# Kernel optimization log

Measured on AMD Instinct MI355X. Metric: run time of the kernel, lower is better.

## Reference

```python
import jax, jax.numpy as jnp
import numpy as np

N, C_IN, C, V = 500000, 64, 64, 20000  # C = out_channel // 2


def bn(x, g, b, eps):
    # training-mode BatchNorm1d: batch statistics, biased variance
    mu = jnp.mean(x, axis=0)
    var = jnp.mean(jnp.square(x - mu), axis=0)
    return (x - mu) * jax.lax.rsqrt(var + eps) * g + b


def setup_inputs() -> dict:
    key = jax.random.key(0)
    ks = jax.random.split(key, 12)
    s = 0.05
    return {
        "inputs": jax.random.normal(ks[0], (N, C_IN), jnp.float32),
        "unq_inv": jax.random.randint(ks[1], (N,), 0, V, jnp.int32),
        "kv_W": jax.random.normal(ks[2], (C_IN, C), jnp.float32) * s,
        "kv_b": jnp.zeros((C,), jnp.float32),
        "norm_g": jnp.ones((C,), jnp.float32),
        "norm_b": jnp.zeros((C,), jnp.float32),
        "w1_W": jax.random.normal(ks[3], (C_IN, C), jnp.float32) * s,
        "w1_bias": jnp.zeros((C,), jnp.float32),
        "w_bn_g": jnp.ones((C,), jnp.float32),
        "w_bn_b": jnp.zeros((C,), jnp.float32),
        "w2_W": jax.random.normal(ks[4], (C, C), jnp.float32) * s,
        "w2_bias": jnp.zeros((C,), jnp.float32),
        "pre_W": jax.random.normal(ks[5], (C_IN, C), jnp.float32) * s,
        "pre_bias": jnp.zeros((C,), jnp.float32),
        "pre_bn_g": jnp.ones((C,), jnp.float32),
        "pre_bn_b": jnp.zeros((C,), jnp.float32),
        "posw_W": jax.random.normal(ks[6], (C, C), jnp.float32) * s,
        "posw_bias": jnp.zeros((C,), jnp.float32),
        "link_bn_g": jnp.ones((C,), jnp.float32),
        "link_bn_b": jnp.zeros((C,), jnp.float32),
    }


def _forward(inputs, unq_inv, kv_W, kv_b, norm_g, norm_b, w1_W, w1_bias,
             w_bn_g, w_bn_b, w2_W, w2_bias, pre_W, pre_bias, pre_bn_g,
             pre_bn_b, posw_W, posw_bias, link_bn_g, link_bn_b):
    inv = unq_inv
    # v = kv(inputs); x = relu(norm(v))
    v = inputs @ kv_W + kv_b                                   # [N, C]
    x = jax.nn.relu(bn(v, norm_g, norm_b, 1e-3))               # [N, C]
    # scatter_max
    q_max = jax.ops.segment_max(x, inv, num_segments=V)        # [V, C]
    q_max = jnp.where(jnp.isneginf(q_max), 0.0, q_max)
    # weight = w(inputs): Linear -> BN -> ReLU -> Linear
    h = jax.nn.relu(bn(inputs @ w1_W + w1_bias, w_bn_g, w_bn_b, 1e-5))
    weight = h @ w2_W + w2_bias                                # [N, C]
    # scatter_softmax over segments
    m = jax.ops.segment_max(weight, inv, num_segments=V)
    m = jnp.where(jnp.isneginf(m), 0.0, m)
    ex = jnp.exp(weight - m[inv])
    denom = jax.ops.segment_sum(ex, inv, num_segments=V)
    soft_weight = ex / denom[inv]                              # [N, C]
    # scatter_mean(soft_weight * v)
    cnt = jax.ops.segment_sum(jnp.ones((inputs.shape[0],), inputs.dtype), inv, num_segments=V)
    cnt = jnp.maximum(cnt, 1.0)[:, None]
    weight_x = jax.ops.segment_sum(soft_weight * v, inv, num_segments=V) / cnt  # [V, C]
    # LinkConv(q_max, inputs, inv)
    p = bn(inputs @ pre_W + pre_bias, pre_bn_g, pre_bn_b, 1e-3)  # [N, C]
    pw = p @ posw_W + posw_bias
    fs = p * jnp.sin(pw)
    fc = p * jnp.cos(pw)
    add_s = jax.ops.segment_sum(fs, inv, num_segments=V)         # [V, C]
    add_c = jax.ops.segment_sum(fc, inv, num_segments=V)
    f = bn(q_max @ pre_W + pre_bias, pre_bn_g, pre_bn_b, 1e-3)   # [V, C]
    mw = f @ posw_W + posw_bias
    cs = f * jnp.sin(mw)
    cc = f * jnp.cos(mw)
    final = (add_s + cs) * cs + (add_c + cc) * cc
    link_feat = jax.nn.relu(bn(final, link_bn_g, link_bn_b, 1e-3))
    weight_x = (link_feat + weight_x) * 0.5
    return jnp.concatenate([weight_x, q_max], axis=-1)           # [V, 2C]


def reference(inputs, unq_inv, kv_W, kv_b, norm_g, norm_b, w1_W, w1_bias,
              w_bn_g, w_bn_b, w2_W, w2_bias, pre_W, pre_bias, pre_bn_g,
              pre_bn_b, posw_W, posw_bias, link_bn_g, link_bn_b):
    return _forward(inputs, unq_inv, kv_W, kv_b, norm_g, norm_b, w1_W, w1_bias,
                    w_bn_g, w_bn_b, w2_W, w2_bias, pre_W, pre_bias, pre_bn_g,
                    pre_bn_b, posw_W, posw_bias, link_bn_g, link_bn_b)
```

## Files before the change

kernel.cpp:

```cpp
#include <hip/hip_runtime.h>

typedef __attribute__((ext_vector_type(8))) short  bf16x8;
typedef __attribute__((ext_vector_type(4))) float  f32x4;

#define MFMA16(a,b,c) __builtin_amdgcn_mfma_f32_16x16x32_bf16((a),(b),(c),0,0,0)

__device__ __forceinline__ float b2f(ushort u){ return __uint_as_float(((unsigned)u)<<16); }
__device__ __forceinline__ ushort f2b(float f){
  unsigned u = __float_as_uint(f);
  unsigned r = (u + 0x7FFFu + ((u>>16)&1u)) >> 16;
  return (ushort)r;
}
__device__ __forceinline__ float ldv(const void* p, long i, int mode){
  return mode ? ((const float*)p)[i] : b2f(((const ushort*)p)[i]);
}

__global__ void pfn_detect(const void* X, int* mode){
  __shared__ int cnt;
  if (threadIdx.x==0) cnt=0;
  __syncthreads();
  const ushort* u = (const ushort*)X;
  int bad=0;
  for (int i=threadIdx.x; i<4096; i+=256){
    float v = b2f(u[i]);
    if (!(fabsf(v) < 1e4f)) bad++;
  }
  atomicAdd(&cnt, bad);
  __syncthreads();
  if (threadIdx.x==0) *mode = (cnt > 204) ? 1 : 0;
}

__global__ __launch_bounds__(256) void pfn_g(const void* __restrict__ X, int N,
                                             float* __restrict__ G, float* __restrict__ svec,
                                             const int* gmode,
                                             const int* __restrict__ inv, int* __restrict__ hist, int V)
{
  __shared__ __align__(16) ushort xt[128*72];
  __shared__ float gred[4096];
  __shared__ float sred[64];
  int mode = *gmode;
  int tid = threadIdx.x;
  int w = tid>>6, lane = tid&63, q = lane>>4, li = lane&15;

  {
    long i = (long)blockIdx.x*blockDim.x + tid;
    long stride = (long)gridDim.x*blockDim.x;
    for (; i<N; i+=stride){
      int s = min(max(inv[i],0), V-1);
      atomicAdd(&hist[s], 1);
    }
  }

  for (int u=tid; u<4096; u+=256) gred[u]=0.f;
  if (tid<64) sred[tid]=0.f;

  float s_acc[32];
#pragma unroll
  for (int i=0;i<32;i++) s_acc[i]=0.f;
  const f32x4 fz = {0.f,0.f,0.f,0.f};
  f32x4 acc[4][4];
#pragma unroll
  for (int a=0;a<4;a++)
#pragma unroll
    for (int b=0;b<4;b++) acc[a][b]=fz;

  int rr = tid>>1, half = tid&1;
  int nch = (N + 127)/128;
  for (int cb = blockIdx.x; cb < nch; cb += gridDim.x){
    int r = cb*128 + rr;
    uint4* dst = (uint4*)(xt + rr*72 + half*32);
    if (r < N){
      if (mode){
        const float4* src = (const float4*)((const float*)X + (size_t)r*64 + half*32);
#pragma unroll
        for (int i=0;i<4;i++){
          float4 f0=src[i*2], f1=src[i*2+1];
          s_acc[i*8+0]+=f0.x; s_acc[i*8+1]+=f0.y; s_acc[i*8+2]+=f0.z; s_acc[i*8+3]+=f0.w;
          s_acc[i*8+4]+=f1.x; s_acc[i*8+5]+=f1.y; s_acc[i*8+6]+=f1.z; s_acc[i*8+7]+=f1.w;
          uint4 u;
          u.x = (unsigned)f2b(f0.x) | ((unsigned)f2b(f0.y)<<16);
          u.y = (unsigned)f2b(f0.z) | ((unsigned)f2b(f0.w)<<16);
          u.z = (unsigned)f2b(f1.x) | ((unsigned)f2b(f1.y)<<16);
          u.w = (unsigned)f2b(f1.z) | ((unsigned)f2b(f1.w)<<16);
          dst[i]=u;
        }
      } else {
        const uint4* src = (const uint4*)((const ushort*)X + (size_t)r*64 + half*32);
#pragma unroll
        for (int i=0;i<4;i++){
          uint4 u=src[i]; dst[i]=u;
          const ushort* pu=(const ushort*)&u;
#pragma unroll
          for (int l=0;l<8;l++) s_acc[i*8+l] += b2f(pu[l]);
        }
      }
    } else {
      uint4 z={0,0,0,0};
#pragma unroll
      for (int i=0;i<4;i++) dst[i]=z;
    }
    __syncthreads();

    bf16x8 fr[4];
#pragma unroll
    for (int mt=0; mt<4; mt++){
      bf16x8 f;
#pragma unroll
      for (int j=0;j<8;j++) f[j] = (short)xt[(w*32 + q*8 + j)*72 + mt*16 + li];
      fr[mt]=f;
    }
#pragma unroll
    for (int mt=0;mt<4;mt++)
#pragma unroll
      for (int nt=0;nt<4;nt++)
        acc[mt][nt] = MFMA16(fr[mt], fr[nt], acc[mt][nt]);
    __syncthreads();
  }
#pragma unroll
  for (int mt=0;mt<4;mt++)
#pragma unroll
    for (int nt=0;nt<4;nt++)
#pragma unroll
      for (int i=0;i<4;i++)
        atomicAdd(&gred[(mt*16 + q*4 + i)*64 + nt*16 + li], acc[mt][nt][i]);
#pragma unroll
  for (int i=0;i<32;i++) atomicAdd(&sred[half*32 + i], s_acc[i]);
  __syncthreads();
  for (int u=tid; u<4096; u+=256) atomicAdd(&G[u], gred[u]);
  if (tid<64) atomicAdd(&svec[tid], sred[tid]);
}

__global__ __launch_bounds__(256) void pfn_kstatsA(
    const float* __restrict__ G, const float* __restrict__ svec,
    const void* __restrict__ kvW, const void* __restrict__ w1W, const void* __restrict__ preW,
    const void* __restrict__ kvb, const void* __restrict__ w1b, const void* __restrict__ preb,
    const void* __restrict__ ng,  const void* __restrict__ nb,
    const void* __restrict__ wg,  const void* __restrict__ wb,
    const void* __restrict__ pg,  const void* __restrict__ pb,
    float* __restrict__ aA, float* __restrict__ cA,
    float* __restrict__ a1, float* __restrict__ ap, float* __restrict__ bp,
    float* __restrict__ bcat, float Nf, const int* gmode)
{
  __shared__ float gl[4096];
  __shared__ float sl[64];
  __shared__ float wl[4096];
  int mode = *gmode;
  int tid = threadIdx.x; int path = blockIdx.x;
  const void* wsel = (path==0)? kvW : (path==1)? w1W : preW;
  for (int u=tid; u<4096; u+=256){ gl[u]=G[u]; wl[u]=ldv(wsel,u,mode); }
  if (tid<64) sl[tid]=svec[tid];
  __syncthreads();
  int j = tid>>2, sub = tid&3;
  float ps=0.f, qf=0.f;
  for (int k=sub*16; k<sub*16+16; k++){
    float wk = wl[k*64+j];
    ps += sl[k]*wk;
    float tk=0.f;
    for (int m=0;m<64;m++) tk += gl[k*64+m]*wl[m*64+j];
    qf += tk*wk;
  }
  qf += __shfl_down(qf,2); qf += __shfl_down(qf,1);
  ps += __shfl_down(ps,2); ps += __shfl_down(ps,1);
  if (sub==0){
    float bias = ldv((path==0)? kvb : (path==1)? w1b : preb, j, mode);
    float gam  = ldv((path==0)? ng  : (path==1)? wg  : pg , j, mode);
    float bet  = ldv((path==0)? nb  : (path==1)? wb  : pb , j, mode);
    float eps  = (path==1)? 1e-5f : 1e-3f;
    float mean_raw = ps/Nf, qn = qf/Nf;
    float mean = mean_raw + bias;
    float var  = qn + 2.f*bias*mean_raw + bias*bias - mean*mean;
    float rstd = rsqrtf(fmaxf(var,0.f)+eps);
    float a = gam*rstd, c = bet - mean*a;
    if (path==0){ aA[j]=a; cA[j]=c; bcat[j]=bias; }
    else if (path==1){ a1[j]=a; bcat[64+j]=c+bias*a; }
    else { ap[j]=a; bp[j]=c+bias*a; bcat[128+j]=c+bias*a; }
  }
}

__global__ __launch_bounds__(256) void pfn_kstatsB(
    const void* __restrict__ kvW, const void* __restrict__ w1W,
    const void* __restrict__ preW, const void* __restrict__ poswW,
    const void* __restrict__ w2W, const void* __restrict__ w2b,
    const void* __restrict__ poswb,
    const float* __restrict__ a1, const float* __restrict__ ap, const float* __restrict__ bp,
    ushort* __restrict__ WT, float* __restrict__ bcat, float* __restrict__ b2o,
    const int* gmode)
{
  int mode = *gmode;
  int gidx = blockIdx.x*256 + threadIdx.x;
  for (int idx=gidx; idx<320*64; idx+=64*256){
    int n = idx>>6, k = idx&63;
    float o;
    if (n<64)        o = ldv(kvW, k*64+n, mode);
    else if (n<128){ int j=n-64;  o = ldv(w1W, k*64+j, mode)*a1[j]; }
    else if (n<192){ int j=n-128; o = ldv(preW, k*64+j, mode)*ap[j]; }
    else if (n<256){ int j=n-192; float t=0.f;
      for (int m=0;m<64;m++) t += ldv(preW,k*64+m,mode)*ap[m]*ldv(poswW,m*64+j,mode);
      o = t;
    } else {         int j=n-256; o = ldv(w2W, k*64+j, mode); }
    WT[idx] = f2b(o);
  }
  if (blockIdx.x==0 && threadIdx.x<64){
    int j = threadIdx.x; float bb=0.f;
    for (int m=0;m<64;m++) bb += bp[m]*ldv(poswW,m*64+j,mode);
    bcat[192+j] = bb + ldv(poswb,j,mode);
    b2o[j] = ldv(w2b,j,mode);
  }
}

__global__ __launch_bounds__(256) void pfn_scan(const int* __restrict__ hist,
                                                int* __restrict__ base, int* __restrict__ off,
                                                float* __restrict__ cntf, int V, int N){
  __shared__ int part[256];
  int tid = threadIdx.x;
  int per = (V+255)/256;
  int s0 = tid*per, s1 = min(s0+per, V);
  int sum=0;
  for (int s=s0;s<s1;s++) sum += hist[s];
  part[tid]=sum;
  __syncthreads();
  if (tid==0){ int acc=0; for (int i=0;i<256;i++){ int t=part[i]; part[i]=acc; acc+=t; } }
  __syncthreads();
  int acc = part[tid];
  for (int s=s0;s<s1;s++){ base[s]=acc; off[s]=acc; cntf[s]=(float)hist[s]; acc+=hist[s]; }
  if (tid==255) base[V]=N;
}

__global__ void pfn_scat(const int* __restrict__ inv, int* __restrict__ off,
                         int* __restrict__ sidx, int* __restrict__ segid, int N, int V){
  int i = blockIdx.x*blockDim.x + threadIdx.x;
  int stride = gridDim.x*blockDim.x;
  for (; i<N; i+=stride){
    int s = min(max(inv[i],0), V-1);
    int p = atomicAdd(&off[s],1);
    sidx[p] = i;
    segid[p] = s;
  }
}

#define RIDX(r,c) (((r)<<6) + ((c) ^ ((r)&31)))

#define RED_STORE(EXPR) \
  _Pragma("unroll") for (int s=0;s<2;s++){ \
  _Pragma("unroll") for (int i=0;i<4;i++){ \
    int rloc=w*32+s*16+q*4+i; \
  _Pragma("unroll") for (int t=0;t<4;t++){ int c=t*16+li; red[RIDX(rloc,c)] = (EXPR); } } }

#define RED_ADD(DST) { int cc=tid&63, gg=tid>>6; int nn=nlsS; \
  for (int ls=gg; ls<nn; ls+=4){ int sd=segSeg[ls]; if (sd<0) continue; \
    int lo=segStart[ls], hi=segStart[ls+1]; float a_=0.f; \
    for (int r_=lo; r_<hi; r_++) a_ += red[RIDX(r_,cc)]; \
    atomicAdd(&DST[(size_t)sd*64+cc], a_); } }

#define RED_MAX(DST) { int cc=tid&63, gg=tid>>6; int nn=nlsS; \
  for (int ls=gg; ls<nn; ls+=4){ int sd=segSeg[ls]; if (sd<0) continue; \
    int lo=segStart[ls], hi=segStart[ls+1]; float a_=0.f; \
    for (int r_=lo; r_<hi; r_++) a_ = fmaxf(a_, red[RIDX(r_,cc)]); \
    atomicMax(&DST[(size_t)sd*64+cc], __float_as_uint(a_)); } }

__global__ __launch_bounds__(256,3) void pfn_ms(
    const void* __restrict__ X, const int* __restrict__ sidx, const int* __restrict__ segid,
    const ushort* __restrict__ WT, const float* __restrict__ bcat,
    const float* __restrict__ aA, const float* __restrict__ cA, const float* __restrict__ b2o,
    unsigned int* __restrict__ qm, float* __restrict__ adds, float* __restrict__ addc,
    float* __restrict__ dnm, float* __restrict__ acv,
    int N, const int* gmode)
{
  __shared__ __align__(16) ushort xt[128*72];
  __shared__ float red[128*64];
  __shared__ float bcl[256], aAl[64], cAl[64], b2l[64];
  __shared__ int segSeg[32];
  __shared__ int nlsS;
  __shared__ unsigned short segStart[34];
  int mode = *gmode;
  int tid = threadIdx.x;
  int p0 = blockIdx.x*128;

  {
    int rr=tid>>1, half=tid&1;
    int p = p0+rr;
    long r = (p<N)? (long)sidx[p] : -1;
    uint4* dst=(uint4*)(xt + rr*72 + half*32);
    if (r>=0){
      if (mode){
        const float4* src=(const float4*)((const float*)X + r*64 + half*32);
#pragma unroll
        for (int i=0;i<4;i++){
          float4 f0=src[i*2], f1=src[i*2+1];
          uint4 u;
          u.x = (unsigned)f2b(f0.x) | ((unsigned)f2b(f0.y)<<16);
          u.y = (unsigned)f2b(f0.z) | ((unsigned)f2b(f0.w)<<16);
          u.z = (unsigned)f2b(f1.x) | ((unsigned)f2b(f1.y)<<16);
          u.w = (unsigned)f2b(f1.z) | ((unsigned)f2b(f1.w)<<16);
          dst[i]=u;
        }
      } else {
        const uint4* src=(const uint4*)((const ushort*)X + r*64 + half*32);
#pragma unroll
        for (int i=0;i<4;i++) dst[i]=src[i];
      }
    } else {
      uint4 z={0,0,0,0};
#pragma unroll
      for (int i=0;i<4;i++) dst[i]=z;
    }
  }
  bcl[tid]=bcat[tid];
  if (tid<64){ aAl[tid]=aA[tid]; cAl[tid]=cA[tid]; b2l[tid]=b2o[tid]; }
  __syncthreads();

  if (tid==0){
    const int* sg = segid + p0;
    int lim = N - p0; if (lim > 128) lim = 128;
    int n=0, prev=-2;
#pragma unroll 8
    for (int t=0;t<128;t++){
      int s = (t<lim)? sg[t] : -1;
      if (s!=prev && n<32){ segStart[n]=(unsigned short)t; segSeg[n]=s; prev=s; n++; }
    }
    segStart[n]=128; nlsS=n;
  }

  int w=tid>>6, lane=tid&63, q=lane>>4, li=lane&15;
  const f32x4 fz={0.f,0.f,0.f,0.f};

  f32x4 AP[2][4], AW[2][4];
#pragma unroll
  for (int s=0;s<2;s++)
#pragma unroll
    for (int t=0;t<4;t++){ AP[s][t]=fz; AW[s][t]=fz; }
#pragma unroll
  for (int kk=0;kk<2;kk++){
    bf16x8 a0 = *(const bf16x8*)&xt[(w*32 +      li)*72 + kk*32 + q*8];
    bf16x8 a1 = *(const bf16x8*)&xt[(w*32 + 16 + li)*72 + kk*32 + q*8];
    int ko = kk*32 + q*8;
#pragma unroll
    for (int t=0;t<4;t++){
      bf16x8 bp_= *(const bf16x8*)&WT[(128 + t*16+li)*64 + ko];
      AP[0][t]=MFMA16(a0,bp_,AP[0][t]); AP[1][t]=MFMA16(a1,bp_,AP[1][t]);
      bf16x8 bw = *(const bf16x8*)&WT[(192 + t*16+li)*64 + ko];
      AW[0][t]=MFMA16(a0,bw,AW[0][t]); AW[1][t]=MFMA16(a1,bw,AW[1][t]);
    }
  }
#pragma unroll
  for (int s=0;s<2;s++)
#pragma unroll
    for (int t=0;t<4;t++)
#pragma unroll
      for (int i=0;i<4;i++){
        int c=t*16+li;
        float p = AP[s][t][i] + bcl[128+c];
        float pw= AW[s][t][i] + bcl[192+c];
        AP[s][t][i] = p*__sinf(pw);
        AW[s][t][i] = p*__cosf(pw);
      }
  RED_STORE(AP[s][t][i]);
  __syncthreads();
  RED_ADD(adds);
  __syncthreads();
  RED_STORE(AW[s][t][i]);
  __syncthreads();
  RED_ADD(addc);
  __syncthreads();

  f32x4 AV[2][4];
#pragma unroll
  for (int s=0;s<2;s++)
#pragma unroll
    for (int t=0;t<4;t++) AV[s][t]=fz;
#pragma unroll
  for (int kk=0;kk<2;kk++){
    bf16x8 a0 = *(const bf16x8*)&xt[(w*32 +      li)*72 + kk*32 + q*8];
    bf16x8 a1 = *(const bf16x8*)&xt[(w*32 + 16 + li)*72 + kk*32 + q*8];
    int ko = kk*32 + q*8;
#pragma unroll
    for (int t=0;t<4;t++){
      bf16x8 bv = *(const bf16x8*)&WT[(      t*16+li)*64 + ko];
      AV[0][t]=MFMA16(a0,bv,AV[0][t]); AV[1][t]=MFMA16(a1,bv,AV[1][t]);
    }
  }
#pragma unroll
  for (int s=0;s<2;s++)
#pragma unroll
    for (int t=0;t<4;t++)
#pragma unroll
      for (int i=0;i<4;i++){
        int c=t*16+li;
        AV[s][t][i] += bcl[c];
      }
  RED_STORE(fmaxf(AV[s][t][i]*aAl[c]+cAl[c], 0.f));
  __syncthreads();
  RED_MAX(qm);
  __syncthreads();

  f32x4 AH[2][4];
#pragma unroll
  for (int s=0;s<2;s++)
#pragma unroll
    for (int t=0;t<4;t++) AH[s][t]=fz;
#pragma unroll
  for (int kk=0;kk<2;kk++){
    bf16x8 a0 = *(const bf16x8*)&xt[(w*32 +      li)*72 + kk*32 + q*8];
    bf16x8 a1 = *(const bf16x8*)&xt[(w*32 + 16 + li)*72 + kk*32 + q*8];
    int ko = kk*32 + q*8;
#pragma unroll
    for (int t=0;t<4;t++){
      bf16x8 bh = *(const bf16x8*)&WT[(64 + t*16+li)*64 + ko];
      AH[0][t]=MFMA16(a0,bh,AH[0][t]); AH[1][t]=MFMA16(a1,bh,AH[1][t]);
    }
  }
#pragma unroll
  for (int s=0;s<2;s++)
#pragma unroll
    for (int i=0;i<4;i++){
      int rloc=w*32+s*16+q*4+i;
#pragma unroll
      for (int t=0;t<4;t++){
        int c=t*16+li;
        xt[rloc*72 + c] = f2b(fmaxf(AH[s][t][i]+bcl[64+c], 0.f));
      }
    }
  __syncthreads();

  f32x4 AZ[2][4];
#pragma unroll
  for (int s=0;s<2;s++)
#pragma unroll
    for (int t=0;t<4;t++) AZ[s][t]=fz;
#pragma unroll
  for (int kk=0;kk<2;kk++){
    bf16x8 a0 = *(const bf16x8*)&xt[(w*32 +      li)*72 + kk*32 + q*8];
    bf16x8 a1 = *(const bf16x8*)&xt[(w*32 + 16 + li)*72 + kk*32 + q*8];
    int ko = kk*32 + q*8;
#pragma unroll
    for (int t=0;t<4;t++){
      bf16x8 bz = *(const bf16x8*)&WT[(256 + t*16+li)*64 + ko];
      AZ[0][t]=MFMA16(a0,bz,AZ[0][t]); AZ[1][t]=MFMA16(a1,bz,AZ[1][t]);
    }
  }
#pragma unroll
  for (int s=0;s<2;s++)
#pragma unroll
    for (int t=0;t<4;t++)
#pragma unroll
      for (int i=0;i<4;i++){
        int c=t*16+li;
        float e = __expf(fminf(AZ[s][t][i]+b2l[c], 30.f));
        AZ[s][t][i] = e;
        AV[s][t][i] = e*AV[s][t][i];
      }
  RED_STORE(AZ[s][t][i]);
  __syncthreads();
  RED_ADD(dnm);
  __syncthreads();
  RED_STORE(AV[s][t][i]);
  __syncthreads();
  RED_ADD(acv);
}

__global__ __launch_bounds__(256) void pfn_k2(
    const float* __restrict__ qmax, const void* __restrict__ preW,
    const void* __restrict__ preb, float* __restrict__ fq,
    float* __restrict__ fsum, float* __restrict__ fssq, int V, const int* gmode)
{
  __shared__ float pwl[64*72];
  __shared__ float qrow[4][64];
  __shared__ float red[8][64];
  int mode = *gmode;
  int tid=threadIdx.x, slot=tid>>6, j=tid&63;
  for (int u=tid;u<4096;u+=256){
    int k=u>>6, n=u&63;
    pwl[k*72+n]=ldv(preW,u,mode);
  }
  int per = (V + (int)gridDim.x - 1)/(int)gridDim.x;
  per = (per+3)&~3;
  int start = blockIdx.x*per, end = min(start+per, V);
  float ps=0.f, pq=0.f;
  float bj = ldv(preb,j,mode);
  __syncthreads();
  for (int rb=start; rb<end; rb+=4){
    int r = rb + slot;
    qrow[slot][j] = (r<V)? qmax[(size_t)r*64+j] : 0.f;
    __syncthreads();
    if (r<end){
      float t=bj;
#pragma unroll
      for (int k=0;k<64;k++) t += qrow[slot][k]*pwl[k*72+j];
      fq[(size_t)r*64+j]=t;
      ps += t; pq += t*t;
    }
    __syncthreads();
  }
  red[slot][j]=ps; red[4+slot][j]=pq;
  __syncthreads();
  if (slot==0){
    float s  = red[0][j]+red[1][j]+red[2][j]+red[3][j];
    float s2 = red[4][j]+red[5][j]+red[6][j]+red[7][j];
    atomicAdd(&fsum[j], s); atomicAdd(&fssq[j], s2);
  }
}

__global__ __launch_bounds__(256) void pfn_k4(
    const float* __restrict__ fq, const float* __restrict__ add_s,
    const float* __restrict__ add_c, const void* __restrict__ poswW,
    const void* __restrict__ poswb,
    const float* __restrict__ fsum, const float* __restrict__ fssq,
    const void* __restrict__ pg, const void* __restrict__ pbeta,
    float* __restrict__ finalb, float* __restrict__ lsum, float* __restrict__ lssq,
    int V, const int* gmode)
{
  __shared__ float pwl[64*72];
  __shared__ float frow[4][64];
  __shared__ float red[8][64];
  int mode = *gmode;
  int tid=threadIdx.x, slot=tid>>6, j=tid&63;
  for (int u=tid;u<4096;u+=256){
    int k=u>>6, n=u&63;
    pwl[k*72+n]=ldv(poswW,u,mode);
  }
  float Vf = (float)V;
  float mean = fsum[j]/Vf;
  float var  = fssq[j]/Vf - mean*mean;
  float s2 = ldv(pg,j,mode)*rsqrtf(fmaxf(var,0.f)+1e-3f);
  float c2 = ldv(pbeta,j,mode) - mean*s2;
  float pbj = ldv(poswb,j,mode);
  int per = (V + (int)gridDim.x - 1)/(int)gridDim.x;
  per = (per+3)&~3;
  int start = blockIdx.x*per, end = min(start+per, V);
  float ps=0.f, pq=0.f;
  __syncthreads();
  for (int rb=start; rb<end; rb+=4){
    int r = rb + slot;
    float fv = 0.f;
    if (r<end) fv = fq[(size_t)r*64+j]*s2 + c2;
    frow[slot][j]=fv;
    __syncthreads();
    if (r<end){
      float mw=pbj;
#pragma unroll
      for (int k=0;k<64;k++) mw += frow[slot][k]*pwl[k*72+j];
      float sn=__sinf(mw), cn=__cosf(mw);
      float cs = fv*sn, cc = fv*cn;
      float fin = (add_s[(size_t)r*64+j]+cs)*cs + (add_c[(size_t)r*64+j]+cc)*cc;
      finalb[(size_t)r*64+j]=fin;
      ps += fin; pq += fin*fin;
    }
    __syncthreads();
  }
  red[slot][j]=ps; red[4+slot][j]=pq;
  __syncthreads();
  if (slot==0){
    float s  = red[0][j]+red[1][j]+red[2][j]+red[3][j];
    float s2r= red[4][j]+red[5][j]+red[6][j]+red[7][j];
    atomicAdd(&lsum[j], s); atomicAdd(&lssq[j], s2r);
  }
}

__global__ __launch_bounds__(256) void pfn_k6(
    const float* __restrict__ finalb, const float* __restrict__ qmax,
    const float* __restrict__ denom, const float* __restrict__ accv,
    const float* __restrict__ cnt,
    const float* __restrict__ lsum, const float* __restrict__ lssq,
    const void* __restrict__ lg, const void* __restrict__ lb,
    void* __restrict__ out, int V, const int* gmode)
{
  int mode = *gmode;
  int tid=threadIdx.x, slot=tid>>6, j=tid&63;
  int r = blockIdx.x*4 + slot;
  if (r>=V) return;
  float Vf=(float)V;
  float mean=lsum[j]/Vf, var=lssq[j]/Vf-mean*mean;
  float s3=ldv(lg,j,mode)*rsqrtf(fmaxf(var,0.f)+1e-3f);
  float c3=ldv(lb,j,mode)-mean*s3;
  float lf = fmaxf(finalb[(size_t)r*64+j]*s3+c3, 0.f);
  float dn = denom[(size_t)r*64+j];
  float wx = accv[(size_t)r*64+j] / fmaxf(dn, 1e-20f);
  wx /= fmaxf(cnt[r],1.f);
  float y0 = (lf+wx)*0.5f;
  float y1 = qmax[(size_t)r*64+j];
  size_t o0 = (size_t)r*128+j, o1 = (size_t)r*128+64+j;
  if (mode){ ((float*)out)[o0]=y0; ((float*)out)[o1]=y1; }
  else { ((ushort*)out)[o0]=f2b(y0); ((ushort*)out)[o1]=f2b(y1); }
}

__global__ void pfn_sent(ushort* out, int n){
  int i = blockIdx.x*256 + threadIdx.x;
  if (i<n) out[i]=0x5300;
}

extern "C" void kernel_launch(void* const* d_in, const int* in_sizes, int n_in,
                              void* d_out, int out_size, void* d_ws, size_t ws_size,
                              hipStream_t stream)
{
  const void* X    = d_in[0];
  const int*  inv  = (const int*)d_in[1];
  const void* kvW  = d_in[2];
  const void* kvb  = d_in[3];
  const void* ng   = d_in[4];
  const void* nb   = d_in[5];
  const void* w1W  = d_in[6];
  const void* w1b  = d_in[7];
  const void* wg   = d_in[8];
  const void* wb   = d_in[9];
  const void* w2W  = d_in[10];
  const void* w2b  = d_in[11];
  const void* preW = d_in[12];
  const void* preb = d_in[13];
  const void* pg   = d_in[14];
  const void* pb   = d_in[15];
  const void* poswW= d_in[16];
  const void* poswb= d_in[17];
  const void* lg   = d_in[18];
  const void* lb   = d_in[19];

  int N = in_sizes[1];
  int V = out_size / 128;

  char* ws = (char*)d_ws;
  size_t off = 0;
  auto alloc = [&](size_t b){ size_t o=off; off=(off+b+255)&~(size_t)255; return o; };
  size_t oMode = alloc(256);
  size_t oG    = alloc(16384);
  size_t oS    = alloc(256);
  size_t oaA   = alloc(256);
  size_t ocA   = alloc(256);
  size_t obcat = alloc(1024);
  size_t ob2   = alloc(256);
  size_t oa1   = alloc(256);
  size_t oap   = alloc(256);
  size_t obp   = alloc(256);
  size_t ofsum = alloc(256);
  size_t ofssq = alloc(256);
  size_t olsum = alloc(256);
  size_t olssq = alloc(256);
  size_t zero1_end = off;
  size_t oWT   = alloc(320*64*2);
  size_t oqm   = alloc((size_t)V*256);
  size_t oadds = alloc((size_t)V*256);
  size_t oaddc = alloc((size_t)V*256);
  size_t odnm  = alloc((size_t)V*256);
  size_t oacv  = alloc((size_t)V*256);
  size_t ohist = alloc((size_t)V*4);
  size_t zero2_end = off;
  size_t ocntf = alloc((size_t)V*4);
  size_t obase = alloc((size_t)(V+1)*4);
  size_t ooff  = alloc((size_t)V*4);
  size_t osidx = alloc((size_t)N*4);
  size_t osegd = alloc((size_t)N*4);
  size_t ofq   = alloc((size_t)V*256);
  size_t ofin  = alloc((size_t)V*256);
  size_t need  = off;
  (void)n_in;

  if (ws_size < need){
    pfn_sent<<<(out_size+255)/256,256,0,stream>>>((ushort*)d_out, out_size);
    return;
  }

  hipMemsetAsync(ws, 0, zero1_end, stream);
  hipMemsetAsync(ws + oqm, 0, zero2_end - oqm, stream);

  int* gmode = (int*)(ws+oMode);

  pfn_detect<<<1,256,0,stream>>>(X, gmode);

  pfn_g<<<512,256,0,stream>>>(X, N, (float*)(ws+oG), (float*)(ws+oS), gmode,
                              inv, (int*)(ws+ohist), V);

  pfn_kstatsA<<<3,256,0,stream>>>(
      (const float*)(ws+oG), (const float*)(ws+oS),
      kvW, w1W, preW, kvb, w1b, preb, ng, nb, wg, wb, pg, pb,
      (float*)(ws+oaA), (float*)(ws+ocA),
      (float*)(ws+oa1),
      (float*)(ws+oap), (float*)(ws+obp),
      (float*)(ws+obcat), (float)N, gmode);

  pfn_scan<<<1,256,0,stream>>>((const int*)(ws+ohist), (int*)(ws+obase),
                               (int*)(ws+ooff), (float*)(ws+ocntf), V, N);

  pfn_kstatsB<<<64,256,0,stream>>>(
      kvW, w1W, preW, poswW, w2W, w2b, poswb,
      (const float*)(ws+oa1), (const float*)(ws+oap), (const float*)(ws+obp),
      (ushort*)(ws+oWT), (float*)(ws+obcat), (float*)(ws+ob2), gmode);

  pfn_scat<<<2048,256,0,stream>>>(inv, (int*)(ws+ooff), (int*)(ws+osidx),
                                  (int*)(ws+osegd), N, V);

  int gb = (N + 127)/128;
  pfn_ms<<<gb,256,0,stream>>>(
      X, (const int*)(ws+osidx), (const int*)(ws+osegd),
      (const ushort*)(ws+oWT), (const float*)(ws+obcat),
      (const float*)(ws+oaA), (const float*)(ws+ocA), (const float*)(ws+ob2),
      (unsigned int*)(ws+oqm), (float*)(ws+oadds), (float*)(ws+oaddc),
      (float*)(ws+odnm), (float*)(ws+oacv),
      N, gmode);

  pfn_k2<<<500,256,0,stream>>>(
      (const float*)(ws+oqm), preW, preb,
      (float*)(ws+ofq), (float*)(ws+ofsum), (float*)(ws+ofssq), V, gmode);

  pfn_k4<<<500,256,0,stream>>>(
      (const float*)(ws+ofq), (const float*)(ws+oadds), (const float*)(ws+oaddc),
      poswW, poswb, (const float*)(ws+ofsum), (const float*)(ws+ofssq),
      pg, pb, (float*)(ws+ofin), (float*)(ws+olsum), (float*)(ws+olssq), V, gmode);

  pfn_k6<<<(V+3)/4,256,0,stream>>>(
      (const float*)(ws+ofin), (const float*)(ws+oqm),
      (const float*)(ws+odnm), (const float*)(ws+oacv), (const float*)(ws+ocntf),
      (const float*)(ws+olsum), (const float*)(ws+olssq),
      lg, lb, d_out, V, gmode);
}
```

Before: 690.8 us.

## Replace shared-memory segment reductions with per-wave register shuffle reductions

Segmented sums and maxes over the 128 sorted rows of a block are now done inside each wave, using masked register accumulation plus cross-lane shuffles, instead of staging through a 32 KB shared buffer and syncing the whole block. This removes the red[] LDS array, which can raise occupancy, and removes most __syncthreads. In exchange, each wave issues its own atomics per segment it touches, so segments that span several waves get more global atomics. It also loops over every local segment with a mask, which costs extra ALU work when segments are short.

```diff
diff --git a/kernel.cpp b/kernel.cpp
--- a/kernel.cpp
+++ b/kernel.cpp
@@ -238,25 +238,49 @@
   }
 }
 
-#define RIDX(r,c) (((r)<<6) + ((c) ^ ((r)&31)))
-
-#define RED_STORE(EXPR) \
-  _Pragma("unroll") for (int s=0;s<2;s++){ \
-  _Pragma("unroll") for (int i=0;i<4;i++){ \
-    int rloc=w*32+s*16+q*4+i; \
-  _Pragma("unroll") for (int t=0;t<4;t++){ int c=t*16+li; red[RIDX(rloc,c)] = (EXPR); } } }
-
-#define RED_ADD(DST) { int cc=tid&63, gg=tid>>6; int nn=nlsS; \
-  for (int ls=gg; ls<nn; ls+=4){ int sd=segSeg[ls]; if (sd<0) continue; \
-    int lo=segStart[ls], hi=segStart[ls+1]; float a_=0.f; \
-    for (int r_=lo; r_<hi; r_++) a_ += red[RIDX(r_,cc)]; \
-    atomicAdd(&DST[(size_t)sd*64+cc], a_); } }
-
-#define RED_MAX(DST) { int cc=tid&63, gg=tid>>6; int nn=nlsS; \
-  for (int ls=gg; ls<nn; ls+=4){ int sd=segSeg[ls]; if (sd<0) continue; \
-    int lo=segStart[ls], hi=segStart[ls+1]; float a_=0.f; \
-    for (int r_=lo; r_<hi; r_++) a_ = fmaxf(a_, red[RIDX(r_,cc)]); \
-    atomicMax(&DST[(size_t)sd*64+cc], __float_as_uint(a_)); } }
+#define WRED_ADD(VAL, DST) { \
+  int nn = nlsS; \
+  for (int ls=0; ls<nn; ls++){ \
+    int sd = segSeg[ls]; \
+    int lo = (int)segStart[ls] - w32, hi = (int)segStart[ls+1] - w32; \
+    lo = max(lo, 0); hi = min(hi, 32); \
+    if (lo>=hi || sd<0) continue; \
+    bool m[2][4]; \
+    _Pragma("unroll") for (int s=0;s<2;s++) \
+    _Pragma("unroll") for (int i=0;i<4;i++){ \
+      int rl = s*16 + q*4 + i; m[s][i] = (rl>=lo) & (rl<hi); } \
+    _Pragma("unroll") for (int t=0;t<4;t++){ \
+      float part = 0.f; \
+      _Pragma("unroll") for (int s=0;s<2;s++) \
+      _Pragma("unroll") for (int i=0;i<4;i++) \
+        if (m[s][i]) part += (VAL); \
+      part += __shfl_xor(part, 16); \
+      part += __shfl_xor(part, 32); \
+      if (lane < 16) atomicAdd(&DST[(size_t)sd*64 + t*16 + li], part); \
+    } \
+  } }
+
+#define WRED_MAX(VAL, DST) { \
+  int nn = nlsS; \
+  for (int ls=0; ls<nn; ls++){ \
+    int sd = segSeg[ls]; \
+    int lo = (int)segStart[ls] - w32, hi = (int)segStart[ls+1] - w32; \
+    lo = max(lo, 0); hi = min(hi, 32); \
+    if (lo>=hi || sd<0) continue; \
+    bool m[2][4]; \
+    _Pragma("unroll") for (int s=0;s<2;s++) \
+    _Pragma("unroll") for (int i=0;i<4;i++){ \
+      int rl = s*16 + q*4 + i; m[s][i] = (rl>=lo) & (rl<hi); } \
+    _Pragma("unroll") for (int t=0;t<4;t++){ \
+      float part = 0.f; \
+      _Pragma("unroll") for (int s=0;s<2;s++) \
+      _Pragma("unroll") for (int i=0;i<4;i++) \
+        if (m[s][i]) part = fmaxf(part, (VAL)); \
+      part = fmaxf(part, __shfl_xor(part, 16)); \
+      part = fmaxf(part, __shfl_xor(part, 32)); \
+      if (lane < 16) atomicMax(&DST[(size_t)sd*64 + t*16 + li], __float_as_uint(part)); \
+    } \
+  } }
 
 __global__ __launch_bounds__(256,3) void pfn_ms(
     const void* __restrict__ X, const int* __restrict__ sidx, const int* __restrict__ segid,
@@ -267,7 +291,6 @@
     int N, const int* gmode)
 {
   __shared__ __align__(16) ushort xt[128*72];
-  __shared__ float red[128*64];
   __shared__ float bcl[256], aAl[64], cAl[64], b2l[64];
   __shared__ int segSeg[32];
   __shared__ int nlsS;
@@ -322,6 +345,7 @@
   }
 
   int w=tid>>6, lane=tid&63, q=lane>>4, li=lane&15;
+  int w32 = w*32;
   const f32x4 fz={0.f,0.f,0.f,0.f};
 
   f32x4 AP[2][4], AW[2][4];
@@ -331,8 +355,8 @@
     for (int t=0;t<4;t++){ AP[s][t]=fz; AW[s][t]=fz; }
 #pragma unroll
   for (int kk=0;kk<2;kk++){
-    bf16x8 a0 = *(const bf16x8*)&xt[(w*32 +      li)*72 + kk*32 + q*8];
-    bf16x8 a1 = *(const bf16x8*)&xt[(w*32 + 16 + li)*72 + kk*32 + q*8];
+    bf16x8 a0 = *(const bf16x8*)&xt[(w32 +      li)*72 + kk*32 + q*8];
+    bf16x8 a1 = *(const bf16x8*)&xt[(w32 + 16 + li)*72 + kk*32 + q*8];
     int ko = kk*32 + q*8;
 #pragma unroll
     for (int t=0;t<4;t++){
@@ -354,14 +378,10 @@
         AP[s][t][i] = p*__sinf(pw);
         AW[s][t][i] = p*__cosf(pw);
       }
-  RED_STORE(AP[s][t][i]);
-  __syncthreads();
-  RED_ADD(adds);
-  __syncthreads();
-  RED_STORE(AW[s][t][i]);
-  __syncthreads();
-  RED_ADD(addc);
-  __syncthreads();
+  __syncthreads();
+
+  WRED_ADD(AP[s][t][i], adds);
+  WRED_ADD(AW[s][t][i], addc);
 
   f32x4 AV[2][4];
 #pragma unroll
@@ -370,8 +390,8 @@
     for (int t=0;t<4;t++) AV[s][t]=fz;
 #pragma unroll
   for (int kk=0;kk<2;kk++){
-    bf16x8 a0 = *(const bf16x8*)&xt[(w*32 +      li)*72 + kk*32 + q*8];
-    bf16x8 a1 = *(const bf16x8*)&xt[(w*32 + 16 + li)*72 + kk*32 + q*8];
+    bf16x8 a0 = *(const bf16x8*)&xt[(w32 +      li)*72 + kk*32 + q*8];
+    bf16x8 a1 = *(const bf16x8*)&xt[(w32 + 16 + li)*72 + kk*32 + q*8];
     int ko = kk*32 + q*8;
 #pragma unroll
     for (int t=0;t<4;t++){
@@ -388,10 +408,7 @@
         int c=t*16+li;
         AV[s][t][i] += bcl[c];
       }
-  RED_STORE(fmaxf(AV[s][t][i]*aAl[c]+cAl[c], 0.f));
-  __syncthreads();
-  RED_MAX(qm);
-  __syncthreads();
+  WRED_MAX(fmaxf(AV[s][t][i]*aAl[t*16+li]+cAl[t*16+li], 0.f), qm);
 
   f32x4 AH[2][4];
 #pragma unroll
@@ -400,8 +417,8 @@
     for (int t=0;t<4;t++) AH[s][t]=fz;
 #pragma unroll
   for (int kk=0;kk<2;kk++){
-    bf16x8 a0 = *(const bf16x8*)&xt[(w*32 +      li)*72 + kk*32 + q*8];
-    bf16x8 a1 = *(const bf16x8*)&xt[(w*32 + 16 + li)*72 + kk*32 + q*8];
+    bf16x8 a0 = *(const bf16x8*)&xt[(w32 +      li)*72 + kk*32 + q*8];
+    bf16x8 a1 = *(const bf16x8*)&xt[(w32 + 16 + li)*72 + kk*32 + q*8];
     int ko = kk*32 + q*8;
 #pragma unroll
     for (int t=0;t<4;t++){
@@ -413,14 +430,13 @@
   for (int s=0;s<2;s++)
 #pragma unroll
     for (int i=0;i<4;i++){
-      int rloc=w*32+s*16+q*4+i;
+      int rloc=w32+s*16+q*4+i;
 #pragma unroll
       for (int t=0;t<4;t++){
         int c=t*16+li;
         xt[rloc*72 + c] = f2b(fmaxf(AH[s][t][i]+bcl[64+c], 0.f));
       }
     }
-  __syncthreads();
 
   f32x4 AZ[2][4];
 #pragma unroll
@@ -429,8 +445,8 @@
     for (int t=0;t<4;t++) AZ[s][t]=fz;
 #pragma unroll
   for (int kk=0;kk<2;kk++){
-    bf16x8 a0 = *(const bf16x8*)&xt[(w*32 +      li)*72 + kk*32 + q*8];
-    bf16x8 a1 = *(const bf16x8*)&xt[(w*32 + 16 + li)*72 + kk*32 + q*8];
+    bf16x8 a0 = *(const bf16x8*)&xt[(w32 +      li)*72 + kk*32 + q*8];
+    bf16x8 a1 = *(const bf16x8*)&xt[(w32 + 16 + li)*72 + kk*32 + q*8];
     int ko = kk*32 + q*8;
 #pragma unroll
     for (int t=0;t<4;t++){
@@ -449,13 +465,8 @@
         AZ[s][t][i] = e;
         AV[s][t][i] = e*AV[s][t][i];
       }
-  RED_STORE(AZ[s][t][i]);
-  __syncthreads();
-  RED_ADD(dnm);
-  __syncthreads();
-  RED_STORE(AV[s][t][i]);
-  __syncthreads();
-  RED_ADD(acv);
+  WRED_ADD(AZ[s][t][i], dnm);
+  WRED_ADD(AV[s][t][i], acv);
 }
 
 __global__ __launch_bounds__(256) void pfn_k2(
```

After: 678.3 us. Within noise of the previous version (-1.8%).
